# Optimization experiments

Measured on AMD Instinct MI355X. Metric: run time of the kernel, lower is better.

## Reference

```python
import jax, jax.numpy as jnp
import numpy as np

B, T, D, H, K, V, W = 2, 2048, 768, 12, 64, 64, 1024
EPS = 1e-6


def setup_inputs() -> dict:
    key = jax.random.key(0)
    ks = jax.random.split(key, 10)
    std = 0.02
    return {
        "x": jax.random.normal(ks[0], (B, T, D), jnp.float32),
        "gdn_state": jax.random.normal(ks[1], (B, H, K, V), jnp.float32),
        "Wq": jax.random.normal(ks[2], (D, H * K), jnp.float32) * std,
        "Wk": jax.random.normal(ks[3], (D, H * K), jnp.float32) * std,
        "Wv": jax.random.normal(ks[4], (D, H * K), jnp.float32) * std,
        "Wo": jax.random.normal(ks[5], (H * K, D), jnp.float32) * std,
        "Wgq": jax.random.normal(ks[6], (D, H * K), jnp.float32) * std,
        "Wro": jax.random.normal(ks[7], (H * V, D), jnp.float32) * std,
        "Wg": jax.random.normal(ks[8], (D, H), jnp.float32) * std,
        "bg": jnp.full((H,), 1.0, jnp.float32),  # swa_gate_init
        "norm_w": jnp.ones((D,), jnp.float32),
    }


def reference(x, gdn_state, Wq, Wk, Wv, Wo, Wgq, Wro, Wg, bg, norm_w):
    # RMSNorm
    xn = x * jax.lax.rsqrt(jnp.mean(x * x, axis=-1, keepdims=True) + EPS) * norm_w

    def proj(w):  # (B,T,D)@(D,HK) -> (B,H,T,K)
        return (xn @ w).reshape(B, T, H, K).transpose(0, 2, 1, 3)

    q, k, v = proj(Wq), proj(Wk), proj(Wv)
    scale = K ** -0.5

    scores = jnp.einsum("bhqk,bhsk->bhqs", q, k) * scale  # (B,H,T,T)
    i = jnp.arange(T)[:, None]
    j = jnp.arange(T)[None, :]
    allowed = (j <= i) & (j >= i - W)  # causal sliding window
    scores = jnp.where(allowed, scores, -jnp.inf)
    attn = jax.nn.softmax(scores, axis=-1)

    local = jnp.einsum("bhqs,bhsk->bhqk", attn, v)
    local = local.transpose(0, 2, 1, 3).reshape(B, T, H * K) @ Wo  # (B,T,D)

    # GDN state retrieval
    qg = jax.nn.relu((xn @ Wgq).reshape(B, T, H, K).transpose(0, 2, 1, 3))  # (B,H,T,K)
    retrieved = jnp.einsum("bhkv,bhtk->bhtv", gdn_state, qg)  # (B,H,T,V)
    retrieval = retrieved.transpose(0, 2, 1, 3).reshape(B, T, H * V) @ Wro  # (B,T,D)
    gate = jax.nn.sigmoid(xn @ Wg + bg)  # (B,T,H)
    retrieval = jnp.mean(gate, axis=-1, keepdims=True) * retrieval

    return x + local + retrieval
```

## Files before the change

kernel.cpp:

```cpp
#include <hip/hip_runtime.h>
#include <math.h>
#include <stdint.h>

typedef float f32x4 __attribute__((ext_vector_type(4)));
typedef __bf16 bf16x8 __attribute__((ext_vector_type(8)));
typedef __bf16 bf16x4 __attribute__((ext_vector_type(4)));

constexpr int Bc = 2, Tc = 2048, Dc = 768, Hc = 12, Wc = 1024;
#define CEXP 0.18033688011112042f

__device__ __forceinline__ f32x4 mfma_bf16(bf16x8 a, bf16x8 b, f32x4 c) {
    return __builtin_amdgcn_mfma_f32_16x16x32_bf16(a, b, c, 0, 0, 0);
}
__device__ __forceinline__ void gload16(const void* g, void* l) {
    __builtin_amdgcn_global_load_lds(
        (const __attribute__((address_space(1))) uint32_t*)g,
        (__attribute__((address_space(3))) uint32_t*)l, 16, 0, 0);
}
__device__ __forceinline__ uint32_t pack2(float a, float b) {
    union { __bf16 h[2]; uint32_t u; } x;
    x.h[0] = (__bf16)a; x.h[1] = (__bf16)b; return x.u;
}
__device__ __forceinline__ void s_wait_vm4()   { asm volatile("s_waitcnt vmcnt(4)" ::: "memory"); }
__device__ __forceinline__ void s_wait_vm2()   { asm volatile("s_waitcnt vmcnt(2)" ::: "memory"); }
__device__ __forceinline__ void s_wait_vm0()   { asm volatile("s_waitcnt vmcnt(0)" ::: "memory"); }
__device__ __forceinline__ void s_wait_lgkm0() { asm volatile("s_waitcnt lgkmcnt(0)" ::: "memory"); }
__device__ __forceinline__ void bar()          { __builtin_amdgcn_s_barrier(); }
__device__ __forceinline__ void wait_tiles2(int infl) {
    if (infl >= 2) s_wait_vm4();
    else if (infl == 1) s_wait_vm2();
    else s_wait_vm0();
}

__global__ __launch_bounds__(256) void k_prep_w(
    const float* __restrict__ Wq, const float* __restrict__ Wk,
    const float* __restrict__ Wv, const float* __restrict__ Wgq,
    const float* __restrict__ Wo, const float* __restrict__ Wro,
    __bf16* __restrict__ wTproj, __bf16* __restrict__ wTout)
{
    __shared__ __bf16 ldsT[64][66];
    const int wsel = blockIdx.y;
    const float* srcs[6] = {Wq, Wk, Wv, Wgq, Wo, Wro};
    const float* src = srcs[wsel];
    __bf16* dst; int dstride, koff;
    if (wsel < 4) { dst = wTproj + (size_t)wsel * Dc * Dc; dstride = Dc;  koff = 0; }
    else if (wsel == 4) { dst = wTout; dstride = 1536; koff = 0; }
    else { dst = wTout; dstride = 1536; koff = 768; }
    const float scale = (wsel == 0) ? CEXP : 1.0f;

    int tile = blockIdx.x;
    int tk = tile % 12, tn = tile / 12;
    int k0 = tk * 64, n0 = tn * 64;
    int i = threadIdx.x, rsub = i >> 4, c4 = i & 15;
#pragma unroll
    for (int rep = 0; rep < 4; ++rep) {
        int row = rep * 16 + rsub;
        float4 v = *(const float4*)(src + (size_t)(k0 + row) * Dc + n0 + c4 * 4);
        ldsT[c4 * 4 + 0][row] = (__bf16)(v.x * scale);
        ldsT[c4 * 4 + 1][row] = (__bf16)(v.y * scale);
        ldsT[c4 * 4 + 2][row] = (__bf16)(v.z * scale);
        ldsT[c4 * 4 + 3][row] = (__bf16)(v.w * scale);
    }
    __syncthreads();
#pragma unroll
    for (int rep = 0; rep < 4; ++rep) {
        int n = rep * 16 + rsub;
        bf16x4 o = *(const bf16x4*)&ldsT[n][c4 * 4];
        *(bf16x4*)(dst + (size_t)(n0 + n) * dstride + koff + k0 + c4 * 4) = o;
    }
}

__global__ __launch_bounds__(256) void k_prep_state(
    const float* __restrict__ st, __bf16* __restrict__ stT)
{
    int idx = blockIdx.x * 256 + threadIdx.x;
    int bh = idx >> 12, kk = (idx >> 6) & 63, vv = idx & 63;
    stT[(size_t)bh * 4096 + vv * 64 + kk] = (__bf16)st[idx];
}

__global__ __launch_bounds__(256) void k_prep_wgt(
    const float* __restrict__ Wg, float* __restrict__ WgT)
{
    int i = blockIdx.x * 256 + threadIdx.x;
    int h = i / Dc, d = i - h * Dc;
    WgT[i] = Wg[d * 12 + h];
}

__global__ __launch_bounds__(256) void k_rmsnorm(
    const float* __restrict__ x, const float* __restrict__ norm_w,
    __bf16* __restrict__ xnb)
{
    int row = blockIdx.x, tid = threadIdx.x;
    const float* xr = x + (size_t)row * Dc;
    float4 v = make_float4(0.f, 0.f, 0.f, 0.f);
    float ss = 0.f;
    if (tid < 192) {
        v = ((const float4*)xr)[tid];
        ss = v.x * v.x + v.y * v.y + v.z * v.z + v.w * v.w;
    }
#pragma unroll
    for (int m = 32; m; m >>= 1) ss += __shfl_xor(ss, m, 64);
    __shared__ float red[4];
    if ((tid & 63) == 0) red[tid >> 6] = ss;
    __syncthreads();
    float tot = red[0] + red[1] + red[2] + red[3];
    float rms = rsqrtf(tot * (1.f / 768.f) + 1e-6f);
    if (tid < 192) {
        float4 nw = ((const float4*)norm_w)[tid];
        bf16x4 o;
        o[0] = (__bf16)(v.x * rms * nw.x);
        o[1] = (__bf16)(v.y * rms * nw.y);
        o[2] = (__bf16)(v.z * rms * nw.z);
        o[3] = (__bf16)(v.w * rms * nw.w);
        *(bf16x4*)(xnb + (size_t)row * Dc + tid * 4) = o;
    }
}

__global__ __launch_bounds__(256) void k_gate(
    const __bf16* __restrict__ xnb, const float* __restrict__ WgT,
    const float* __restrict__ bg, float* __restrict__ gmean)
{
    int row = blockIdx.x * 4 + (threadIdx.x >> 6);
    int lane = threadIdx.x & 63;
    const __bf16* xr = xnb + (size_t)row * Dc;
    float p[12];
#pragma unroll
    for (int h = 0; h < 12; ++h) p[h] = 0.f;
    for (int d = lane; d < Dc; d += 64) {
        float xv = (float)xr[d];
#pragma unroll
        for (int h = 0; h < 12; ++h) p[h] += xv * WgT[h * Dc + d];
    }
#pragma unroll
    for (int h = 0; h < 12; ++h) {
#pragma unroll
        for (int m = 32; m; m >>= 1) p[h] += __shfl_xor(p[h], m, 64);
    }
    if (lane == 0) {
        float s = 0.f;
#pragma unroll
        for (int h = 0; h < 12; ++h) s += 1.f / (1.f + expf(-(p[h] + bg[h])));
        gmean[row] = s * (1.f / 12.f);
    }
}

template <int MODE>
__global__ __launch_bounds__(256) void k_gemm(
    const __bf16* __restrict__ A, const __bf16* __restrict__ BT,
    const float* __restrict__ xres, float* __restrict__ outf,
    __bf16* __restrict__ qb, __bf16* __restrict__ kbf,
    __bf16* __restrict__ vtb, __bf16* __restrict__ qgb)
{
    constexpr int BM = (MODE == 0) ? 128 : 64;
    constexpr int BN = (MODE == 0) ? 128 : 64;
    constexpr int KD = (MODE == 0) ? 768 : 1536;
    constexpr int BK = (MODE == 0) ? 32 : 64;
    constexpr int KI = BK / 32;
    constexpr int WM = BM / 2, WN = BN / 2;
    constexpr int MI = WM / 16, NI = WN / 16;
    constexpr int MT = 4096 / BM;
    constexpr int NK = KD / BK;
    constexpr int GR = BK / 8;
    constexpr int ACH = BM * BK / 2048;
    constexpr int BCH = BN * BK / 2048;
    __shared__ __bf16 As[2][BM * BK];
    __shared__ __bf16 Bs[2][BN * BK];
    const int tid = threadIdx.x, w = tid >> 6, lane = tid & 63;
    const int g = lane >> 4, t = lane & 15;
    int id = blockIdx.x, xcd = id & 7, l = id >> 3;
    int nid = xcd * 96 + l;
    int m0 = (nid % MT) * BM, n0 = (nid / MT) * BN;
    const __bf16* Abase = A + (size_t)m0 * KD;
    const __bf16* Bbase = BT + (size_t)n0 * KD;
    const int wrow = (w >> 1) * WM, wcol = (w & 1) * WN;

    auto STAGE = [&](int buf, int k0) {
#pragma unroll
        for (int c = 0; c < ACH; ++c) {
            int chunk = c * 256 + tid, row = chunk / GR, cix = chunk % GR;
            gload16(Abase + (size_t)row * KD + k0 + cix * 8, &As[buf][chunk * 8]);
        }
#pragma unroll
        for (int c = 0; c < BCH; ++c) {
            int chunk = c * 256 + tid, row = chunk / GR, cix = chunk % GR;
            gload16(Bbase + (size_t)row * KD + k0 + cix * 8, &Bs[buf][chunk * 8]);
        }
    };

    f32x4 acc[MI][NI] = {};
    STAGE(0, 0);
    STAGE(1, BK);
    for (int ks = 0; ks < NK; ++ks) {
        if (ks == NK - 1) s_wait_vm0(); else s_wait_vm4();
        bar();
        const __bf16* Ab = As[ks & 1];
        const __bf16* Bb = Bs[ks & 1];
        bf16x8 af[MI][KI], bfr[NI][KI];
#pragma unroll
        for (int kk = 0; kk < KI; ++kk) {
#pragma unroll
            for (int mi = 0; mi < MI; ++mi)
                af[mi][kk] = *(const bf16x8*)(Ab + (wrow + mi * 16 + t) * BK + kk * 32 + g * 8);
#pragma unroll
            for (int ni = 0; ni < NI; ++ni)
                bfr[ni][kk] = *(const bf16x8*)(Bb + (wcol + ni * 16 + t) * BK + kk * 32 + g * 8);
        }
        s_wait_lgkm0();
        __builtin_amdgcn_sched_barrier(0);
        bar();
        if (ks + 2 < NK) STAGE(ks & 1, (ks + 2) * BK);
        __builtin_amdgcn_s_setprio(1);
#pragma unroll
        for (int kk = 0; kk < KI; ++kk)
#pragma unroll
            for (int mi = 0; mi < MI; ++mi)
#pragma unroll
                for (int ni = 0; ni < NI; ++ni)
                    acc[mi][ni] = mfma_bf16(af[mi][kk], bfr[ni][kk], acc[mi][ni]);
        __builtin_amdgcn_s_setprio(0);
    }
    const int region = (MODE == 0) ? (n0 / 768) : 0;
#pragma unroll
    for (int mi = 0; mi < MI; ++mi)
#pragma unroll
        for (int ni = 0; ni < NI; ++ni)
#pragma unroll
            for (int r = 0; r < 4; ++r) {
                int grow = m0 + wrow + mi * 16 + g * 4 + r;
                int gcol = n0 + wcol + ni * 16 + t;
                float v = acc[mi][ni][r];
                if (MODE == 1) {
                    size_t idx = (size_t)grow * Dc + gcol;
                    outf[idx] = xres[idx] + v;
                } else {
                    int c = gcol - region * 768;
                    int h = c >> 6, kd = c & 63;
                    int b = grow >> 11, ti = grow & (Tc - 1);
                    if (region == 0)
                        qb[((size_t)(b * Hc + h) * Tc + ti) * 64 + kd] = (__bf16)v;
                    else if (region == 1) {
                        int kds = kd ^ ((ti & 7) << 3);
                        kbf[((size_t)(b * Hc + h) * Tc + ti) * 64 + kds] = (__bf16)v;
                    } else if (region == 2) {
                        int kap = ti & 63;
                        int rho = (kap & 32) | (((kap >> 2) & 3) << 3) |
                                  (((kap >> 4) & 1) << 2) | (kap & 3);
                        int ts = (ti & ~63) | (rho ^ ((kd & 7) << 3));
                        vtb[((size_t)(b * Hc + h) * 64 + kd) * Tc + ts] = (__bf16)v;
                    } else
                        qgb[((size_t)(b * Hc + h) * Tc + ti) * 64 + kd] = (__bf16)fmaxf(v, 0.f);
                }
            }
}

__global__ __launch_bounds__(512, 6) void k_attn(
    const __bf16* __restrict__ q, const __bf16* __restrict__ k,
    const __bf16* __restrict__ vt, const __bf16* __restrict__ qg,
    const __bf16* __restrict__ stateT, const float* __restrict__ gmean,
    __bf16* __restrict__ ac)
{
    __shared__ __bf16 Ks[3][64 * 64];
    __shared__ __bf16 Vs[3][64 * 64];
    int id = blockIdx.x, xcd = id & 7, l = id >> 3;
    int nid = xcd * 96 + l;
    int sblk = nid & 31, h = (nid >> 5) % Hc, b = nid / (32 * Hc);
    int tid = threadIdx.x;
    int w = tid >> 6, lane = tid & 63;
    int g = lane >> 4, t = lane & 15;
    int q0 = sblk * 64, qw = q0 + (w & 3) * 16;
    const int myPar = w >> 2;
    const __bf16* qb = q + (size_t)(b * Hc + h) * Tc * 64;
    const __bf16* kb = k + (size_t)(b * Hc + h) * Tc * 64;
    const __bf16* vb = vt + (size_t)(b * Hc + h) * 64 * Tc;

    bf16x8 qf0 = *(const bf16x8*)(qb + (size_t)(qw + t) * 64 + g * 8);
    bf16x8 qf1 = *(const bf16x8*)(qb + (size_t)(qw + t) * 64 + 32 + g * 8);

    const int qi = qw + t;
    const int lowB = qi - Wc;
    const int xr = t & 7;

    f32x4 oacc[4] = {};
    float lsum = 0.f;

    const int s_begin = (q0 >= Wc) ? q0 - Wc : 0;
    const int NT = (q0 + 64 - s_begin) >> 6;

    auto STAGE = [&](int buf, int s0) {
        int ch = tid;
        gload16(kb + (size_t)(s0 + (ch >> 3)) * 64 + (ch & 7) * 8, &Ks[buf][ch * 8]);
        gload16(vb + (size_t)(ch >> 3) * Tc + s0 + (ch & 7) * 8, &Vs[buf][ch * 8]);
    };

    STAGE(0, s_begin);
    if (NT > 1) STAGE(1, s_begin + 64);
    if (NT > 2) STAGE(2, s_begin + 128);
    int buf = 0;
    for (int it = 0; it < NT; ++it) {
        int s0 = s_begin + it * 64;
        wait_tiles2(NT - 1 - it);
        bar();
        if ((it & 1) == myPar) {
            const __bf16* Kt = Ks[buf];
            const __bf16* Vt = Vs[buf];
            f32x4 sc[4];
            __builtin_amdgcn_s_setprio(1);
#pragma unroll
            for (int sub = 0; sub < 4; ++sub) {
                const __bf16* kr = Kt + (sub * 16 + t) * 64;
                bf16x8 kA = *(const bf16x8*)(kr + ((g ^ xr) << 3));
                bf16x8 kB = *(const bf16x8*)(kr + (((g + 4) ^ xr) << 3));
                f32x4 s = {};
                s = mfma_bf16(kA, qf0, s);
                s = mfma_bf16(kB, qf1, s);
                sc[sub] = s;
            }
            __builtin_amdgcn_s_setprio(0);
            float pv[4][4];
#pragma unroll
            for (int sub = 0; sub < 4; ++sub)
#pragma unroll
                for (int r = 0; r < 4; ++r) {
                    int kk = s0 + sub * 16 + g * 4 + r;
                    float e = exp2f(sc[sub][r]);
                    float val = (kk <= qi && kk >= lowB) ? e : 0.f;
                    pv[sub][r] = val;
                    lsum += val;
                }
            __builtin_amdgcn_s_setprio(1);
#pragma unroll
            for (int ks = 0; ks < 2; ++ks) {
                union { uint32_t u[4]; bf16x8 v; } pf;
                pf.u[0] = pack2(pv[ks * 2][0], pv[ks * 2][1]);
                pf.u[1] = pack2(pv[ks * 2][2], pv[ks * 2][3]);
                pf.u[2] = pack2(pv[ks * 2 + 1][0], pv[ks * 2 + 1][1]);
                pf.u[3] = pack2(pv[ks * 2 + 1][2], pv[ks * 2 + 1][3]);
#pragma unroll
                for (int n = 0; n < 4; ++n) {
                    const __bf16* vrow = Vt + (n * 16 + t) * 64;
                    bf16x8 vf = *(const bf16x8*)(vrow + ((((ks * 4) + g) ^ xr) << 3));
                    oacc[n] = mfma_bf16(pf.v, vf, oacc[n]);
                }
            }
            __builtin_amdgcn_s_setprio(0);
        }
        s_wait_lgkm0();
        __builtin_amdgcn_sched_barrier(0);
        bar();
        if (it + 3 < NT) STAGE(buf, s0 + 192);
        buf = (buf == 2) ? 0 : buf + 1;
    }
    float* cb = (float*)&Ks[0][0];
    if (w >= 4) {
        float* dst = cb + ((size_t)((w - 4) * 64 + lane)) * 20;
#pragma unroll
        for (int n = 0; n < 4; ++n) *(f32x4*)(dst + n * 4) = oacc[n];
        dst[16] = lsum;
    }
    bar();
    if (w < 4) {
        const float* src = cb + ((size_t)(w * 64 + lane)) * 20;
#pragma unroll
        for (int n = 0; n < 4; ++n) oacc[n] += *(const f32x4*)(src + n * 4);
        lsum += src[16];
        lsum += __shfl_xor(lsum, 16, 64);
        lsum += __shfl_xor(lsum, 32, 64);
        float linv = 1.f / lsum;
        float lq[4];
#pragma unroll
        for (int r = 0; r < 4; ++r) lq[r] = __shfl(linv, g * 4 + r, 64);
#pragma unroll
        for (int n = 0; n < 4; ++n)
#pragma unroll
            for (int r = 0; r < 4; ++r) {
                int qrow = qw + g * 4 + r;
                ac[(size_t)(b * Tc + qrow) * 1536 + h * 64 + n * 16 + t] =
                    (__bf16)(oacc[n][r] * lq[r]);
            }
        const __bf16* qgp = qg + (size_t)(b * Hc + h) * Tc * 64;
        const __bf16* sb = stateT + (size_t)(b * Hc + h) * 4096;
        bf16x8 a0 = *(const bf16x8*)(qgp + (size_t)(qw + t) * 64 + g * 8);
        bf16x8 a1 = *(const bf16x8*)(qgp + (size_t)(qw + t) * 64 + 32 + g * 8);
#pragma unroll
        for (int n = 0; n < 4; ++n) {
            bf16x8 b0 = *(const bf16x8*)(sb + (n * 16 + t) * 64 + g * 8);
            bf16x8 b1 = *(const bf16x8*)(sb + (n * 16 + t) * 64 + 32 + g * 8);
            f32x4 acc2 = {};
            acc2 = mfma_bf16(a0, b0, acc2);
            acc2 = mfma_bf16(a1, b1, acc2);
#pragma unroll
            for (int r = 0; r < 4; ++r) {
                int ti = qw + g * 4 + r;
                float gm = gmean[b * Tc + ti];
                ac[(size_t)(b * Tc + ti) * 1536 + 768 + h * 64 + n * 16 + t] =
                    (__bf16)(acc2[r] * gm);
            }
        }
    }
}

extern "C" void kernel_launch(void* const* d_in, const int* in_sizes, int n_in,
                              void* d_out, int out_size, void* d_ws, size_t ws_size,
                              hipStream_t stream) {
    (void)in_sizes; (void)n_in; (void)out_size; (void)ws_size;
    const float* x     = (const float*)d_in[0];
    const float* gdn   = (const float*)d_in[1];
    const float* Wq    = (const float*)d_in[2];
    const float* Wk    = (const float*)d_in[3];
    const float* Wv    = (const float*)d_in[4];
    const float* Wo    = (const float*)d_in[5];
    const float* Wgq   = (const float*)d_in[6];
    const float* Wro   = (const float*)d_in[7];
    const float* Wg    = (const float*)d_in[8];
    const float* bg    = (const float*)d_in[9];
    const float* normw = (const float*)d_in[10];
    float* out = (float*)d_out;

    char* p = (char*)d_ws;
    auto alloc = [&](size_t bytes) -> char* {
        char* r = p; p += (bytes + 255) & ~(size_t)255; return r;
    };
    constexpr size_t NROW = (size_t)Bc * Tc;
    __bf16* xnb    = (__bf16*)alloc(NROW * Dc * 2);
    __bf16* wTproj = (__bf16*)alloc((size_t)4 * Dc * Dc * 2);
    __bf16* wTout  = (__bf16*)alloc((size_t)Dc * 1536 * 2);
    __bf16* stT    = (__bf16*)alloc((size_t)Bc * Hc * 64 * 64 * 2);
    __bf16* qbuf   = (__bf16*)alloc(NROW * Dc * 2);
    __bf16* kbuf   = (__bf16*)alloc(NROW * Dc * 2);
    __bf16* qgbuf  = (__bf16*)alloc(NROW * Dc * 2);
    __bf16* vtbuf  = (__bf16*)alloc(NROW * Dc * 2);
    __bf16* ac     = (__bf16*)alloc(NROW * 1536 * 2);
    float*  gmean  = (float*)alloc(NROW * 4);
    float*  WgT    = (float*)alloc((size_t)12 * Dc * 4);

    k_prep_w<<<dim3(144, 6), 256, 0, stream>>>(Wq, Wk, Wv, Wgq, Wo, Wro, wTproj, wTout);
    k_prep_state<<<(Bc * Hc * 64 * 64) / 256, 256, 0, stream>>>(gdn, stT);
    k_prep_wgt<<<36, 256, 0, stream>>>(Wg, WgT);
    k_rmsnorm<<<NROW, 256, 0, stream>>>(x, normw, xnb);
    k_gate<<<NROW / 4, 256, 0, stream>>>(xnb, WgT, bg, gmean);

    k_gemm<0><<<768, 256, 0, stream>>>(xnb, wTproj, nullptr, nullptr,
                                       qbuf, kbuf, vtbuf, qgbuf);
    k_attn<<<768, 512, 0, stream>>>(qbuf, kbuf, vtbuf, qgbuf, stT, gmean, ac);
    k_gemm<1><<<768, 256, 0, stream>>>(ac, wTout, x, out,
                                       nullptr, nullptr, nullptr, nullptr);
}
```

Baseline: 129.8 us.

## Use triple-buffered LDS ring to drop second barrier per k-step in GEMM and attention

The GEMM moves to a 3-slot LDS ring for A and B. The attention loop now keeps its existing 3-slot ring two tiles ahead instead of three. In both loops the next tile is issued right after the single top-of-loop barrier, which removes the lgkm wait and the second barrier each iteration. This cuts synchronisation stalls at the cost of more LDS in the GEMM (possible occupancy loss) and a shallower prefetch depth in attention.

```diff
diff --git a/kernel.cpp b/kernel.cpp
--- a/kernel.cpp
+++ b/kernel.cpp
@@ -21,16 +21,10 @@
     union { __bf16 h[2]; uint32_t u; } x;
     x.h[0] = (__bf16)a; x.h[1] = (__bf16)b; return x.u;
 }
-__device__ __forceinline__ void s_wait_vm4()   { asm volatile("s_waitcnt vmcnt(4)" ::: "memory"); }
-__device__ __forceinline__ void s_wait_vm2()   { asm volatile("s_waitcnt vmcnt(2)" ::: "memory"); }
-__device__ __forceinline__ void s_wait_vm0()   { asm volatile("s_waitcnt vmcnt(0)" ::: "memory"); }
-__device__ __forceinline__ void s_wait_lgkm0() { asm volatile("s_waitcnt lgkmcnt(0)" ::: "memory"); }
-__device__ __forceinline__ void bar()          { __builtin_amdgcn_s_barrier(); }
-__device__ __forceinline__ void wait_tiles2(int infl) {
-    if (infl >= 2) s_wait_vm4();
-    else if (infl == 1) s_wait_vm2();
-    else s_wait_vm0();
-}
+__device__ __forceinline__ void s_wait_vm4() { asm volatile("s_waitcnt vmcnt(4)" ::: "memory"); }
+__device__ __forceinline__ void s_wait_vm2() { asm volatile("s_waitcnt vmcnt(2)" ::: "memory"); }
+__device__ __forceinline__ void s_wait_vm0() { asm volatile("s_waitcnt vmcnt(0)" ::: "memory"); }
+__device__ __forceinline__ void bar()        { __builtin_amdgcn_s_barrier(); }
 
 __global__ __launch_bounds__(256) void k_prep_w(
     const float* __restrict__ Wq, const float* __restrict__ Wk,
@@ -163,8 +157,8 @@
     constexpr int GR = BK / 8;
     constexpr int ACH = BM * BK / 2048;
     constexpr int BCH = BN * BK / 2048;
-    __shared__ __bf16 As[2][BM * BK];
-    __shared__ __bf16 Bs[2][BN * BK];
+    __shared__ __bf16 As[3][BM * BK];
+    __shared__ __bf16 Bs[3][BN * BK];
     const int tid = threadIdx.x, w = tid >> 6, lane = tid & 63;
     const int g = lane >> 4, t = lane & 15;
     int id = blockIdx.x, xcd = id & 7, l = id >> 3;
@@ -190,11 +184,17 @@
     f32x4 acc[MI][NI] = {};
     STAGE(0, 0);
     STAGE(1, BK);
+    int bufr = 0;
     for (int ks = 0; ks < NK; ++ks) {
-        if (ks == NK - 1) s_wait_vm0(); else s_wait_vm4();
+        if (ks + 1 < NK) s_wait_vm4(); else s_wait_vm0();
         bar();
-        const __bf16* Ab = As[ks & 1];
-        const __bf16* Bb = Bs[ks & 1];
+        if (ks + 2 < NK) {
+            int ss = bufr + 2; if (ss >= 3) ss -= 3;
+            STAGE(ss, (ks + 2) * BK);
+        }
+        const __bf16* Ab = As[bufr];
+        const __bf16* Bb = Bs[bufr];
+        bufr = (bufr == 2) ? 0 : bufr + 1;
         bf16x8 af[MI][KI], bfr[NI][KI];
 #pragma unroll
         for (int kk = 0; kk < KI; ++kk) {
@@ -205,10 +205,6 @@
             for (int ni = 0; ni < NI; ++ni)
                 bfr[ni][kk] = *(const bf16x8*)(Bb + (wcol + ni * 16 + t) * BK + kk * 32 + g * 8);
         }
-        s_wait_lgkm0();
-        __builtin_amdgcn_sched_barrier(0);
-        bar();
-        if (ks + 2 < NK) STAGE(ks & 1, (ks + 2) * BK);
         __builtin_amdgcn_s_setprio(1);
 #pragma unroll
         for (int kk = 0; kk < KI; ++kk)
@@ -294,15 +290,18 @@
 
     STAGE(0, s_begin);
     if (NT > 1) STAGE(1, s_begin + 64);
-    if (NT > 2) STAGE(2, s_begin + 128);
-    int buf = 0;
+    int bufr = 0;
     for (int it = 0; it < NT; ++it) {
         int s0 = s_begin + it * 64;
-        wait_tiles2(NT - 1 - it);
+        if (it + 1 < NT) s_wait_vm2(); else s_wait_vm0();
         bar();
+        if (it + 2 < NT) {
+            int ss = bufr + 2; if (ss >= 3) ss -= 3;
+            STAGE(ss, s0 + 128);
+        }
         if ((it & 1) == myPar) {
-            const __bf16* Kt = Ks[buf];
-            const __bf16* Vt = Vs[buf];
+            const __bf16* Kt = Ks[bufr];
+            const __bf16* Vt = Vs[bufr];
             f32x4 sc[4];
             __builtin_amdgcn_s_setprio(1);
 #pragma unroll
@@ -344,12 +343,9 @@
             }
             __builtin_amdgcn_s_setprio(0);
         }
-        s_wait_lgkm0();
-        __builtin_amdgcn_sched_barrier(0);
-        bar();
-        if (it + 3 < NT) STAGE(buf, s0 + 192);
-        buf = (buf == 2) ? 0 : buf + 1;
-    }
+        bufr = (bufr == 2) ? 0 : bufr + 1;
+    }
+    bar();
     float* cb = (float*)&Ks[0][0];
     if (w >= 4) {
         float* dst = cb + ((size_t)((w - 4) * 64 + lane)) * 20;
```

Measured after the change: 135.3 us. +4.2%, slower.
